# Performance work log

Hardware: AMD Instinct MI355X
Metric: run time of the kernel (lower is better)

Reference implementation:

```python
import jax, jax.numpy as jnp
import numpy as np

EPS = 1e-5
K = 20
NH = 16
SLOPE = 0.2

def leaky(x):
    return jnp.where(x >= 0, x, SLOPE * x)

def bn(x, g, b, axes):
    # training-mode batch norm (biased variance), channel axis = 1
    m = x.mean(axes, keepdims=True)
    v = x.var(axes, keepdims=True)
    shp = [1] * x.ndim
    shp[1] = -1
    return (x - m) / jnp.sqrt(v + EPS) * g.reshape(shp) + b.reshape(shp)

def efr(x, idx, w, k):
    # x: [B, C, N]; idx: flat global gather indices [B*N*k]; w: [C_out, 2C+1]
    B, C, N = x.shape
    xt = x.transpose(0, 2, 1).reshape(B * N, C)
    feature = xt[idx].reshape(B, N, k, C)            # gathered neighbors
    xc = xt.reshape(B, N, 1, C)
    fmean = feature.mean(-1, keepdims=True)          # [B,N,k,1]
    f = jnp.concatenate([feature - xc, fmean, jnp.broadcast_to(xc, feature.shape)], axis=3)
    return jnp.einsum('bnkc,oc->bonk', f, w)         # 1x1 conv -> [B,C_out,N,k]


def setup_inputs() -> dict:
    key = jax.random.key(0)
    ks = jax.random.split(key, 24)
    B, N = 8, 4096
    IN_CH, FEAT_CH, OUT_CH = 6, 64, 64
    d = {}
    d['points'] = jax.random.normal(ks[0], (B, IN_CH // 2, N), dtype=jnp.float32)
    d['feat'] = jax.random.normal(ks[1], (B, FEAT_CH // 2, N), dtype=jnp.float32)
    d['idx'] = jax.random.randint(ks[2], (B * N * K,), 0, B * N)
    s = 0.1
    d['w_efr_p'] = jax.random.normal(ks[3], (IN_CH, IN_CH + 1), dtype=jnp.float32) * s
    d['w_efr_f'] = jax.random.normal(ks[4], (FEAT_CH, FEAT_CH + 1), dtype=jnp.float32) * s
    d['w_q'] = jax.random.normal(ks[5], (FEAT_CH, FEAT_CH // 2), dtype=jnp.float32) * s
    d['g_q'] = jnp.ones((FEAT_CH,), jnp.float32)
    d['b_q'] = jnp.zeros((FEAT_CH,), jnp.float32)
    d['w_pos1'] = jax.random.normal(ks[6], (IN_CH, IN_CH // 2), dtype=jnp.float32) * s
    d['g_pos1'] = jnp.ones((IN_CH,), jnp.float32)
    d['b_pos1'] = jnp.zeros((IN_CH,), jnp.float32)
    d['w_pos2'] = jax.random.normal(ks[7], (FEAT_CH, IN_CH), dtype=jnp.float32) * s
    d['w_attn'] = jax.random.normal(ks[8], (NH * IN_CH, FEAT_CH), dtype=jnp.float32) * s
    d['g1'] = jnp.ones((NH,), jnp.float32)
    d['b1'] = jnp.zeros((NH,), jnp.float32)
    d['w_lin'] = jax.random.normal(ks[9], (OUT_CH, NH), dtype=jnp.float32) * s
    d['g_lin'] = jnp.ones((OUT_CH,), jnp.float32)
    d['b_lin'] = jnp.zeros((OUT_CH,), jnp.float32)
    d['w_res'] = jax.random.normal(ks[10], (OUT_CH, FEAT_CH), dtype=jnp.float32) * s
    d['g_res'] = jnp.ones((OUT_CH,), jnp.float32)
    d['b_res'] = jnp.zeros((OUT_CH,), jnp.float32)
    return d


def reference(points, feat, idx, w_efr_p, w_efr_f, w_q, g_q, b_q,
              w_pos1, g_pos1, b_pos1, w_pos2, w_attn, g1, b1,
              w_lin, g_lin, b_lin, w_res, g_res, b_res):
    B, _, N = points.shape
    knn_points = efr(points, idx, w_efr_p, K)   # [B,6,N,K]
    knn_feat = efr(feat, idx, w_efr_f, K)       # [B,64,N,K]
    x_q = leaky(bn(jnp.einsum('bcn,oc->bon', feat, w_q), g_q, b_q, (0, 2)))
    pos = leaky(bn(jnp.einsum('bcn,oc->bon', points, w_pos1), g_pos1, b_pos1, (0, 2)))
    pos = pos[:, :, :, None] - knn_points       # [B,6,N,K]
    pos = jnp.einsum('bcnk,oc->bonk', pos, w_pos2)  # [B,64,N,K]
    attn = x_q[:, :, :, None] - knn_feat + pos
    attn = jax.nn.softmax(attn / float(np.sqrt(knn_feat.shape[1])), axis=-1)
    attn = jnp.einsum('bcnk,oc->bonk', attn, w_attn)  # [B,NH*6,N,K]
    attn5 = attn.transpose(0, 2, 3, 1).reshape(B, N, K, NH, -1)  # [B,N,K,NH,6]
    y = jnp.einsum('bnkhc,bcnk->bhnk', attn5, knn_points)        # [B,NH,N,K]
    y = leaky(bn(y, g1, b1, (0, 2, 3)))
    y = bn(jnp.einsum('bcnk,oc->bonk', y, w_lin), g_lin, b_lin, (0, 2, 3))
    res = bn(jnp.einsum('bcnk,oc->bonk', knn_feat, w_res), g_res, b_res, (0, 2, 3))
    y = leaky(y + res)
    return y.max(axis=-1)                        # [B,64,N]
```

## Files before the change

kernel.cpp:

```cpp
#include <hip/hip_runtime.h>

#define KNN 20
#define NN 4096
#define NPTS 32768
#define PPW 8

using short8 = __attribute__((ext_vector_type(8))) short;
using f32x4v = __attribute__((ext_vector_type(4))) float;
using uint4v = __attribute__((ext_vector_type(4))) unsigned int;

__device__ __forceinline__ float lrelu(float x){ return x >= 0.f ? x : 0.2f*x; }
__device__ __forceinline__ unsigned short f2b(float x){
    union { float f; unsigned u; } v; v.f = x;
    unsigned r = v.u + 0x7FFFu + ((v.u >> 16) & 1u);
    return (unsigned short)(r >> 16);
}
__device__ __forceinline__ float b2f(unsigned h){
    union { unsigned u; float f; } v; v.u = h << 16; return v.f;
}
#define WSYNC() do { asm volatile("s_waitcnt lgkmcnt(0)" ::: "memory"); __builtin_amdgcn_sched_barrier(0); } while(0)

__device__ __forceinline__ int fslot(int fragi, int klocal, int gp){
    return fragi*1024 + (((klocal) + ((gp)<<4)) ^ ((gp)*5))*16;
}

__global__ void kprep(const float* __restrict__ weff, const float* __restrict__ wattn,
                      const float* __restrict__ wres,
                      unsigned short* __restrict__ packW, float* __restrict__ wdiff,
                      float* __restrict__ w32t)
{
    int t = threadIdx.x;
    for (int q = t; q < 1536; q += 256){
        int f = q >> 6, l = q & 63;
        const float* W; int n, rowlen, koff;
        if (f < 4){ W = weff; rowlen = 65; n = f*16 + (l&15); koff = 0; }
        else if (f < 16){ W = wattn; rowlen = 64; int ff = f-4; n = (ff>>1)*16 + (l&15); koff = (ff&1)*32; }
        else { W = wres; rowlen = 64; int ff = f-16; n = (ff>>1)*16 + (l&15); koff = (ff&1)*32; }
        #pragma unroll
        for (int j=0;j<8;j++){
            int k = koff + (j>=4?16:0) + 4*(l>>4) + (j&3);
            packW[(size_t)(f*64+l)*8 + j] = f2b(W[n*rowlen + k]);
        }
    }
    for (int q = t; q < 2048; q += 256){
        int c = q >> 5, j = q & 31;
        wdiff[q] = weff[c*65 + 33 + j] - weff[c*65 + j];
    }
    if (t < 64) w32t[t] = weff[t*65 + 32];
}

__global__ void __launch_bounds__(256) k0_prep(
    const float* __restrict__ pts, const float* __restrict__ feat,
    const float* __restrict__ wq, const float* __restrict__ wpos1,
    const float* __restrict__ wefp, const float* __restrict__ wdiff,
    unsigned short* __restrict__ ft16, float* __restrict__ pt4,
    unsigned short* __restrict__ qp16, float* __restrict__ pp,
    unsigned short* __restrict__ base16, float* __restrict__ bpp,
    float* __restrict__ qsum, float* __restrict__ qsq,
    float* __restrict__ psum, float* __restrict__ psq)
{
    __shared__ float swq[2048];
    __shared__ float swd[2048];
    __shared__ float red[4][64], red2[4][64];
    int tid = threadIdx.x;
    for (int m=tid;m<2048;m+=256){ swq[m]=wq[m]; swd[m]=wdiff[m]; }
    __syncthreads();
    int r = blockIdx.x*256 + tid;
    int b = r >> 12, n = r & 4095;
    float p0 = pts[((size_t)b*3+0)*NN+n];
    float p1 = pts[((size_t)b*3+1)*NN+n];
    float p2 = pts[((size_t)b*3+2)*NN+n];
    float pm = (p0+p1+p2)*(1.f/3.f);
    *(float4*)(pt4 + (size_t)r*4) = make_float4(p0,p1,p2,pm);
    float f[32];
    #pragma unroll
    for (int c=0;c<32;c++) f[c] = feat[((size_t)b*32+c)*NN+n];
    #pragma unroll
    for (int c=0;c<32;c+=2){
        unsigned pk = (unsigned)f2b(f[c]) | ((unsigned)f2b(f[c+1])<<16);
        *(unsigned*)(ft16 + (size_t)r*32 + c) = pk;
    }
    float q[64];
    for (int o=0;o<64;o++){
        float a=0.f;
        #pragma unroll
        for (int c=0;c<32;c++) a += swq[o*32+c]*f[c];
        q[o]=a;
    }
    for (int o=0;o<64;o+=2){
        unsigned pk = (unsigned)f2b(q[o]) | ((unsigned)f2b(q[o+1])<<16);
        *(unsigned*)(qp16 + (size_t)r*64 + o) = pk;
    }
    int lane = tid & 63, wvv = tid>>6;
    for (int o=0;o<64;o++){
        float s=q[o], s2=q[o]*q[o];
        for (int d=1; d<64; d<<=1){ s += __shfl_xor(s,d); s2 += __shfl_xor(s2,d); }
        if (lane==0){ red[wvv][o]=s; red2[wvv][o]=s2; }
    }
    __syncthreads();
    if (tid<64){
        atomicAdd(qsum+tid, red[0][tid]+red[1][tid]+red[2][tid]+red[3][tid]);
        atomicAdd(qsq+tid, red2[0][tid]+red2[1][tid]+red2[2][tid]+red2[3][tid]);
    }
    for (int o=0;o<64;o++){
        float a=0.f;
        #pragma unroll
        for (int c=0;c<32;c++) a += swd[o*32+c]*f[c];
        q[o]=a;
    }
    for (int o=0;o<64;o+=2){
        unsigned pk = (unsigned)f2b(q[o]) | ((unsigned)f2b(q[o+1])<<16);
        *(unsigned*)(base16 + (size_t)r*64 + o) = pk;
    }
    float pr[8];
    #pragma unroll
    for (int o=0;o<6;o++) pr[o] = wpos1[o*3]*p0 + wpos1[o*3+1]*p1 + wpos1[o*3+2]*p2;
    pr[6]=0.f; pr[7]=0.f;
    *(float4*)(pp+(size_t)r*8)   = make_float4(pr[0],pr[1],pr[2],pr[3]);
    *(float4*)(pp+(size_t)r*8+4) = make_float4(pr[4],pr[5],pr[6],pr[7]);
    __syncthreads();
    for (int o=0;o<6;o++){
        float s=pr[o], s2=pr[o]*pr[o];
        for (int d=1;d<64;d<<=1){ s += __shfl_xor(s,d); s2 += __shfl_xor(s2,d); }
        if (lane==0){ red[wvv][o]=s; red2[wvv][o]=s2; }
    }
    __syncthreads();
    if (tid<6){
        atomicAdd(psum+tid, red[0][tid]+red[1][tid]+red[2][tid]+red[3][tid]);
        atomicAdd(psq+tid, red2[0][tid]+red2[1][tid]+red2[2][tid]+red2[3][tid]);
    }
    #pragma unroll
    for (int j=0;j<6;j++)
        bpp[(size_t)r*8+j] = p0*(wefp[j*7+4]-wefp[j*7]) + p1*(wefp[j*7+5]-wefp[j*7+1])
                           + p2*(wefp[j*7+6]-wefp[j*7+2]);
    bpp[(size_t)r*8+6]=0.f; bpp[(size_t)r*8+7]=0.f;
}

__global__ void k1_paramsA(
    const float* __restrict__ qsum, const float* __restrict__ qsq,
    const float* __restrict__ psum, const float* __restrict__ psq,
    const float* __restrict__ gq, const float* __restrict__ bq,
    const float* __restrict__ gp, const float* __restrict__ bp,
    float* __restrict__ bnq_a, float* __restrict__ bnq_c,
    float* __restrict__ bnp_a, float* __restrict__ bnp_c)
{
    int t = threadIdx.x;
    const float inv = 1.f/32768.f;
    if (t < 64){
        float m = qsum[t]*inv; float v = qsq[t]*inv - m*m;
        float a = gq[t]*rsqrtf(v + 1e-5f);
        bnq_a[t] = a; bnq_c[t] = bq[t] - m*a;
    }
    if (t < 6){
        float m = psum[t]*inv; float v = psq[t]*inv - m*m;
        float a = gp[t]*rsqrtf(v + 1e-5f);
        bnp_a[t] = a; bnp_c[t] = bp[t] - m*a;
    }
}

#define ARENA 12544
#define ANB   0
#define ATR   2048
#define KFR   6272
#define SFM   10368
#define SSKP  10496
#define SIDX  11136
#define YST   11776

__global__ void __launch_bounds__(256, 3) k2_main(
    const unsigned short* __restrict__ ft16, const float* __restrict__ pt4,
    const unsigned short* __restrict__ qp16, const float* __restrict__ pp,
    const unsigned short* __restrict__ base16, const float* __restrict__ bpp,
    const int* __restrict__ idx,
    const float* __restrict__ wefp, const float* __restrict__ wpos2,
    const unsigned short* __restrict__ packW, const float* __restrict__ w32t,
    const float* __restrict__ bnq_a, const float* __restrict__ bnq_c,
    const float* __restrict__ bnp_a, const float* __restrict__ bnp_c,
    unsigned short* __restrict__ yv, unsigned short* __restrict__ rf,
    float* __restrict__ yslot, float* __restrict__ rslot)
{
    __shared__ __align__(16) char smem_[4*ARENA];
    const int tid = threadIdx.x;
    const int l = tid & 63, wv = tid >> 6;
    const int lo = l & 15, g = l >> 4;
    char* S = smem_ + wv*ARENA;
    const int srd = (l ^ (g*5))*16;

    float w2r[4][6], w32r[4], bnqa[4], bnqc[4];
    #pragma unroll
    for (int nt=0;nt<4;nt++){
        #pragma unroll
        for (int j=0;j<6;j++) w2r[nt][j] = wpos2[(nt*16+lo)*6+j];
        w32r[nt] = w32t[nt*16+lo];
        bnqa[nt] = bnq_a[nt*16+lo];
        bnqc[nt] = bnq_c[nt*16+lo];
    }
    float bnpa[6], bnpc[6];
    #pragma unroll
    for (int j=0;j<6;j++){ bnpa[j]=bnp_a[j]; bnpc[j]=bnp_c[j]; }

    float ysum=0.f, ysq=0.f;
    float racc[4]={0.f,0.f,0.f,0.f}, rsqa[4]={0.f,0.f,0.f,0.f};

    const int rbase = blockIdx.x*(4*PPW) + wv*PPW;

    *(int*)(S+SIDX+l*4)        = idx[(size_t)rbase*KNN + l];
    *(int*)(S+SIDX+(64+l)*4)   = idx[(size_t)rbase*KNN + 64 + l];
    if (l < 32) *(int*)(S+SIDX+(128+l)*4) = idx[(size_t)rbase*KNN + 128 + l];
    WSYNC();

    uint2 ng0, ng1; uint2 ng2 = make_uint2(0u,0u); float4 ngp4 = make_float4(0,0,0,0);
    unsigned short nqr[4], nbr[4];
    float nppr[6], nbppr[6];
    float xqv[4], basev[4], sp[6];

#define ISSUE(pi_) { \
    int sb = (pi_)*KNN*4; size_t rr = (size_t)(rbase + (pi_)); \
    int i0 = *(const int*)(S+SIDX+sb+(l>>3)*4); \
    int i1 = *(const int*)(S+SIDX+sb+(8+(l>>3))*4); \
    ng0 = *(const uint2*)(ft16 + (size_t)i0*32 + (l&7)*4); \
    ng1 = *(const uint2*)(ft16 + (size_t)i1*32 + (l&7)*4); \
    if (l < 32){ int i2 = *(const int*)(S+SIDX+sb+(16+(l>>3))*4); \
                 ng2 = *(const uint2*)(ft16 + (size_t)i2*32 + (l&7)*4); } \
    if (l < KNN){ int ip = *(const int*)(S+SIDX+sb+l*4); \
                  ngp4 = *(const float4*)(pt4 + (size_t)ip*4); } \
    _Pragma("unroll") for (int nt=0;nt<4;nt++){ \
        nqr[nt] = qp16[rr*64 + nt*16+lo]; nbr[nt] = base16[rr*64 + nt*16+lo]; } \
    _Pragma("unroll") for (int j=0;j<6;j++){ nppr[j] = pp[rr*8+j]; nbppr[j] = bpp[rr*8+j]; } \
    __builtin_amdgcn_sched_barrier(0); \
}

#define STAGE() { \
    float s0 = b2f(ng0.x&0xffffu)+b2f(ng0.x>>16)+b2f(ng0.y&0xffffu)+b2f(ng0.y>>16); \
    float s1 = b2f(ng1.x&0xffffu)+b2f(ng1.x>>16)+b2f(ng1.y&0xffffu)+b2f(ng1.y>>16); \
    float s2 = b2f(ng2.x&0xffffu)+b2f(ng2.x>>16)+b2f(ng2.y&0xffffu)+b2f(ng2.y>>16); \
    s0 += __shfl_xor(s0,1); s0 += __shfl_xor(s0,2); s0 += __shfl_xor(s0,4); \
    s1 += __shfl_xor(s1,1); s1 += __shfl_xor(s1,2); s1 += __shfl_xor(s1,4); \
    s2 += __shfl_xor(s2,1); s2 += __shfl_xor(s2,2); s2 += __shfl_xor(s2,4); \
    if ((l&7)==0){ \
        *(float*)(S+SFM+(l>>3)*4) = s0*(1.f/32.f); \
        *(float*)(S+SFM+(8+(l>>3))*4) = s1*(1.f/32.f); \
        if (l < 32) *(float*)(S+SFM+(16+(l>>3))*4) = s2*(1.f/32.f); \
    } \
    { int kk = l>>3, gp_ = l&3, jb = ((l>>2)&1)*8; \
      *(uint2*)(S + ANB + fslot(0, kk, gp_) + jb) = ng0; \
      *(uint2*)(S + ANB + fslot(0, 8+kk, gp_) + jb) = ng1; \
      if (l < 32) *(uint2*)(S + ANB + fslot(1, kk, gp_) + jb) = ng2; } \
    if (l < KNN){ \
        _Pragma("unroll") for (int j=0;j<6;j++){ \
            float v = nbppr[j] + wefp[j*7]*ngp4.x + wefp[j*7+1]*ngp4.y \
                    + wefp[j*7+2]*ngp4.z + wefp[j*7+3]*ngp4.w; \
            *(float*)(S+SSKP+(l*8+j)*4) = v; } } \
    _Pragma("unroll") for (int nt=0;nt<4;nt++){ \
        xqv[nt] = lrelu(bnqa[nt]*b2f(nqr[nt]) + bnqc[nt]); \
        basev[nt] = b2f(nbr[nt]); } \
    _Pragma("unroll") for (int j=0;j<6;j++) sp[j] = lrelu(bnpa[j]*nppr[j] + bnpc[j]); \
    WSYNC(); \
}

    ISSUE(0);
    STAGE();

    for (int pi=0; pi<PPW; pi++){
        const size_t r = (size_t)(rbase + pi);
        if (pi < PPW-1) ISSUE(pi+1);

        f32x4v C1[2][4];
        #pragma unroll
        for (int mt=0;mt<2;mt++)
            #pragma unroll
            for (int nt=0;nt<4;nt++)
                #pragma unroll
                for (int i=0;i<4;i++) C1[mt][nt][i] = 0.f;
        short8 Af0 = *(const short8*)(S + ANB + 0*1024 + srd);
        short8 Af1 = *(const short8*)(S + ANB + 1*1024 + srd);
        #pragma unroll
        for (int nt=0;nt<4;nt++){
            short8 Bf = *(const short8*)(packW + (size_t)(nt*64 + l)*8);
            C1[0][nt] = __builtin_amdgcn_mfma_f32_16x16x32_bf16(Af0, Bf, C1[0][nt], 0, 0, 0);
            C1[1][nt] = __builtin_amdgcn_mfma_f32_16x16x32_bf16(Af1, Bf, C1[1][nt], 0, 0, 0);
        }
        #pragma unroll
        for (int mt=0;mt<2;mt++){
            #pragma unroll
            for (int i=0;i<4;i++){
                int k = mt*16 + g*4 + i;
                bool valid = (k < KNN);
                int kk = valid ? k : 0;
                float fmk = *(const float*)(S+SFM+kk*4);
                float sk[6];
                #pragma unroll
                for (int j=0;j<6;j++) sk[j] = *(const float*)(S+SSKP+(kk*8+j)*4);
                #pragma unroll
                for (int nt=0;nt<4;nt++){
                    float kf = C1[mt][nt][i] + basev[nt] + w32r[nt]*fmk;
                    if (valid){
                        int fa = fslot(mt*2+(nt>>1), g*4+i, lo>>2) + ((nt&1)*4 + (lo&3))*2;
                        *(unsigned short*)(S + KFR + fa) = f2b(kf);
                    }
                    float pos = 0.f;
                    #pragma unroll
                    for (int j=0;j<6;j++) pos += (sp[j]-sk[j])*w2r[nt][j];
                    C1[mt][nt][i] = valid ? (xqv[nt] - kf + pos)*0.125f : -1e30f;
                }
            }
        }
        #pragma unroll
        for (int nt=0;nt<4;nt++){
            float mx = -1e30f;
            #pragma unroll
            for (int mt=0;mt<2;mt++)
                #pragma unroll
                for (int i=0;i<4;i++) mx = fmaxf(mx, C1[mt][nt][i]);
            mx = fmaxf(mx, __shfl_xor(mx,16));
            mx = fmaxf(mx, __shfl_xor(mx,32));
            float sm = 0.f;
            #pragma unroll
            for (int mt=0;mt<2;mt++)
                #pragma unroll
                for (int i=0;i<4;i++){ float e = __expf(C1[mt][nt][i]-mx); C1[mt][nt][i]=e; sm += e; }
            sm += __shfl_xor(sm,16);
            sm += __shfl_xor(sm,32);
            float inv = 1.f/sm;
            #pragma unroll
            for (int mt=0;mt<2;mt++)
                #pragma unroll
                for (int i=0;i<4;i++){
                    int k = mt*16 + g*4 + i;
                    if (k < KNN){
                        int fa = fslot(mt*2+(nt>>1), g*4+i, lo>>2) + ((nt&1)*4 + (lo&3))*2;
                        *(unsigned short*)(S + ATR + fa) = f2b(C1[mt][nt][i]*inv);
                    }
                }
        }
        WSYNC();
        short8 Aa[2][2];
        #pragma unroll
        for (int mt=0;mt<2;mt++)
            #pragma unroll
            for (int s=0;s<2;s++) Aa[mt][s] = *(const short8*)(S + ATR + (mt*2+s)*1024 + srd);
        f32x4v C2[2][6];
        #pragma unroll
        for (int mt=0;mt<2;mt++)
            #pragma unroll
            for (int nt=0;nt<6;nt++)
                #pragma unroll
                for (int i=0;i<4;i++) C2[mt][nt][i] = 0.f;
        #pragma unroll
        for (int nt=0;nt<6;nt++){
            #pragma unroll
            for (int s=0;s<2;s++){
                short8 Bf = *(const short8*)(packW + (size_t)((4+nt*2+s)*64 + l)*8);
                #pragma unroll
                for (int mt=0;mt<2;mt++)
                    C2[mt][nt] = __builtin_amdgcn_mfma_f32_16x16x32_bf16(Aa[mt][s], Bf, C2[mt][nt], 0, 0, 0);
            }
        }
        WSYNC();
        #pragma unroll
        for (int mt=0;mt<2;mt++)
            #pragma unroll
            for (int nt=0;nt<6;nt++)
                #pragma unroll
                for (int i=0;i<4;i++){
                    int k = mt*16 + g*4 + i;
                    if (k < KNN)
                        *(unsigned short*)(S + ATR + k*208 + (nt*16+lo)*2) = f2b(C2[mt][nt][i]);
                }
        WSYNC();
        #pragma unroll
        for (int it=0; it<5; it++){
            int kq = it*4 + g;
            const char* row = S + ATR + kq*208 + lo*12;
            unsigned d0 = *(const unsigned*)(row);
            unsigned d1 = *(const unsigned*)(row+4);
            unsigned d2 = *(const unsigned*)(row+8);
            float yval = b2f(d0&0xffffu) * (*(const float*)(S+SSKP+(kq*8+0)*4))
                       + b2f(d0>>16)    * (*(const float*)(S+SSKP+(kq*8+1)*4))
                       + b2f(d1&0xffffu)* (*(const float*)(S+SSKP+(kq*8+2)*4))
                       + b2f(d1>>16)    * (*(const float*)(S+SSKP+(kq*8+3)*4))
                       + b2f(d2&0xffffu)* (*(const float*)(S+SSKP+(kq*8+4)*4))
                       + b2f(d2>>16)    * (*(const float*)(S+SSKP+(kq*8+5)*4));
            *(unsigned short*)(S + YST + kq*32 + lo*2) = f2b(yval);
            ysum += yval; ysq += yval*yval;
        }
        short8 Ak[2][2];
        #pragma unroll
        for (int mt=0;mt<2;mt++)
            #pragma unroll
            for (int s=0;s<2;s++) Ak[mt][s] = *(const short8*)(S + KFR + (mt*2+s)*1024 + srd);
        f32x4v C3[2][4];
        #pragma unroll
        for (int mt=0;mt<2;mt++)
            #pragma unroll
            for (int nt=0;nt<4;nt++)
                #pragma unroll
                for (int i=0;i<4;i++) C3[mt][nt][i] = 0.f;
        #pragma unroll
        for (int nt=0;nt<4;nt++){
            #pragma unroll
            for (int s=0;s<2;s++){
                short8 Bf = *(const short8*)(packW + (size_t)((16+nt*2+s)*64 + l)*8);
                #pragma unroll
                for (int mt=0;mt<2;mt++)
                    C3[mt][nt] = __builtin_amdgcn_mfma_f32_16x16x32_bf16(Ak[mt][s], Bf, C3[mt][nt], 0, 0, 0);
            }
        }
        WSYNC();
        #pragma unroll
        for (int mt=0;mt<2;mt++)
            #pragma unroll
            for (int i=0;i<4;i++){
                int k = mt*16 + g*4 + i;
                if (k < KNN){
                    #pragma unroll
                    for (int nt=0;nt<4;nt++){
                        float v = C3[mt][nt][i];
                        *(unsigned short*)(S + ATR + k*144 + (nt*16+lo)*2) = f2b(v);
                        racc[nt] += v; rsqa[nt] += v*v;
                    }
                }
            }
        WSYNC();
        if (l < 40){
            uint4v v = *(const uint4v*)(S + YST + l*16);
            __builtin_nontemporal_store(v, (uint4v*)((char*)yv + r*640 + l*16));
        }
        #pragma unroll
        for (int t=0;t<3;t++){
            int s = t*64 + l;
            if (s < 160){
                int kk = s>>3, pt_ = s&7;
                uint4v v = *(const uint4v*)(S + ATR + kk*144 + pt_*16);
                __builtin_nontemporal_store(v, (uint4v*)((char*)rf + r*2560 + kk*128 + pt_*16));
            }
        }
        if (pi < PPW-1) STAGE();
    }
    ysum += __shfl_xor(ysum,16); ysum += __shfl_xor(ysum,32);
    ysq  += __shfl_xor(ysq,16);  ysq  += __shfl_xor(ysq,32);
    #pragma unroll
    for (int nt=0;nt<4;nt++){
        racc[nt] += __shfl_xor(racc[nt],16); racc[nt] += __shfl_xor(racc[nt],32);
        rsqa[nt] += __shfl_xor(rsqa[nt],16); rsqa[nt] += __shfl_xor(rsqa[nt],32);
    }
    int slot = (blockIdx.x*4 + wv) & 63;
    if (l < 16){
        atomicAdd(yslot + slot*32 + l, ysum);
        #pragma unroll
        for (int nt=0;nt<4;nt++) atomicAdd(rslot + slot*128 + nt*16 + l, racc[nt]);
    } else if (l < 32){
        atomicAdd(yslot + slot*32 + 16 + lo, ysq);
        #pragma unroll
        for (int nt=0;nt<4;nt++) atomicAdd(rslot + slot*128 + 64 + nt*16 + lo, rsqa[nt]);
    }
#undef ISSUE
#undef STAGE
}

__global__ void k3_paramsB(
    const float* __restrict__ yslot, const float* __restrict__ rslot,
    const float* __restrict__ g1, const float* __restrict__ b1,
    const float* __restrict__ gr, const float* __restrict__ br,
    float* __restrict__ bn1_a, float* __restrict__ bn1_c,
    float* __restrict__ bnr_a, float* __restrict__ bnr_c)
{
    __shared__ float sy[32];
    __shared__ float sr[128];
    int t = threadIdx.x;
    float s1 = 0.f;
    if (t < 32){ for (int i=0;i<64;i++) s1 += yslot[(size_t)i*32+t]; }
    float s2 = 0.f;
    for (int i=0;i<64;i++) s2 += rslot[(size_t)i*128+t];
    if (t < 32) sy[t] = s1;
    sr[t] = s2;
    __syncthreads();
    const float inv = 1.f/655360.f;
    if (t < 16){
        float m = sy[t]*inv; float v = sy[16+t]*inv - m*m;
        float a = g1[t]*rsqrtf(v + 1e-5f);
        bn1_a[t] = a; bn1_c[t] = b1[t] - m*a;
    }
    if (t < 64){
        float m = sr[t]*inv; float v = sr[64+t]*inv - m*m;
        float a = gr[t]*rsqrtf(v + 1e-5f);
        bnr_a[t] = a; bnr_c[t] = br[t] - m*a;
    }
}

__global__ void __launch_bounds__(256) k4_linstats(
    const unsigned short* __restrict__ yv,
    const float* __restrict__ bn1_a, const float* __restrict__ bn1_c,
    float* __restrict__ Mslot, float* __restrict__ Sslot)
{
    __shared__ __align__(16) char lds[4*1024];
    const int tid = threadIdx.x, l = tid & 63, wvv = tid >> 6;
    const int lo = l & 15, g = l >> 4;
    char* L = lds + wvv*1024;
    const int h0 = (l&1)*8;
    float a8[8], c8[8];
    #pragma unroll
    for (int j=0;j<8;j++){ a8[j]=bn1_a[h0+j]; c8[j]=bn1_c[h0+j]; }
    short8 ones;
    #pragma unroll
    for (int j=0;j<8;j++) ones[j] = (short)0x3F80;
    f32x4v Macc, Sacc;
    #pragma unroll
    for (int i=0;i<4;i++){ Macc[i]=0.f; Sacc[i]=0.f; }
    const int waveid = blockIdx.x*4 + wvv;
    for (int it=0; it<5; it++){
        size_t s0 = ((size_t)waveid*5 + it)*32;
        uint4 v = *(const uint4*)(yv + s0*16 + l*8);
        unsigned short e0 = v.x&0xffffu, e1 = v.x>>16, e2 = v.y&0xffffu, e3 = v.y>>16;
        unsigned short e4 = v.z&0xffffu, e5 = v.z>>16, e6 = v.w&0xffffu, e7 = v.w>>16;
        float y0 = lrelu(a8[0]*b2f(e0)+c8[0]), y1 = lrelu(a8[1]*b2f(e1)+c8[1]);
        float y2_ = lrelu(a8[2]*b2f(e2)+c8[2]), y3 = lrelu(a8[3]*b2f(e3)+c8[3]);
        float y4 = lrelu(a8[4]*b2f(e4)+c8[4]), y5 = lrelu(a8[5]*b2f(e5)+c8[5]);
        float y6 = lrelu(a8[6]*b2f(e6)+c8[6]), y7 = lrelu(a8[7]*b2f(e7)+c8[7]);
        uint4 o;
        o.x = (unsigned)f2b(y0) | ((unsigned)f2b(y1)<<16);
        o.y = (unsigned)f2b(y2_)| ((unsigned)f2b(y3)<<16);
        o.z = (unsigned)f2b(y4) | ((unsigned)f2b(y5)<<16);
        o.w = (unsigned)f2b(y6) | ((unsigned)f2b(y7)<<16);
        *(uint4*)(L + l*16) = o;
        WSYNC();
        short8 Af;
        #pragma unroll
        for (int j=0;j<8;j++){
            int s = 4*g + (j&3) + ((j>=4)?16:0);
            Af[j] = *(const short*)(L + s*32 + lo*2);
        }
        WSYNC();
        Macc = __builtin_amdgcn_mfma_f32_16x16x32_bf16(Af, Af, Macc, 0, 0, 0);
        Sacc = __builtin_amdgcn_mfma_f32_16x16x32_bf16(ones, Af, Sacc, 0, 0, 0);
    }
    float* Ms = Mslot + (size_t)(waveid&15)*256;
    #pragma unroll
    for (int i=0;i<4;i++) atomicAdd(Ms + (g*4+i)*16 + lo, Macc[i]);
    if (l < 16) atomicAdd(Sslot + (size_t)(waveid&15)*16 + lo, Sacc[0]);
}

__global__ void k5_paramsC(
    const float* __restrict__ Mslot, const float* __restrict__ Sslot,
    const float* __restrict__ wl,
    const float* __restrict__ gl, const float* __restrict__ bl,
    float* __restrict__ bnl_a, float* __restrict__ bnl_c)
{
    __shared__ float Ms[256], Ss[16];
    int t = threadIdx.x;
    float m = 0.f;
    for (int i=0;i<16;i++) m += Mslot[(size_t)i*256+t];
    Ms[t] = m;
    if (t < 16){
        float s = 0.f;
        for (int i=0;i<16;i++) s += Sslot[(size_t)i*16+t];
        Ss[t] = s;
    }
    __syncthreads();
    if (t < 64){
        float w[16];
        #pragma unroll
        for (int h=0;h<16;h++) w[h] = wl[t*16+h];
        float lsum = 0.f;
        #pragma unroll
        for (int h=0;h<16;h++) lsum += w[h]*Ss[h];
        float lsq = 0.f;
        for (int h1=0;h1<16;h1++){
            float acc = 0.f;
            #pragma unroll
            for (int h2=0;h2<16;h2++) acc += Ms[h1*16+h2]*w[h2];
            lsq += w[h1]*acc;
        }
        const float inv = 1.f/655360.f;
        float mean = lsum*inv; float var = lsq*inv - mean*mean;
        float a = gl[t]*rsqrtf(var + 1e-5f);
        bnl_a[t] = a; bnl_c[t] = bl[t] - mean*a;
    }
}

__global__ void __launch_bounds__(256) k6_final(
    const unsigned short* __restrict__ yv, const unsigned short* __restrict__ rf,
    const float* __restrict__ bn1_a, const float* __restrict__ bn1_c,
    const float* __restrict__ wl,
    const float* __restrict__ bnl_a, const float* __restrict__ bnl_c,
    const float* __restrict__ bnr_a, const float* __restrict__ bnr_c,
    float* __restrict__ out)
{
    __shared__ float sy2[4][16*KNN];
    __shared__ float sout[64][17];
    const int tid = threadIdx.x;
    const int w = tid >> 6, o = tid & 63;
    float wlr[16];
    #pragma unroll
    for (int h=0;h<16;h++) wlr[h] = wl[o*16+h];
    const float la = bnl_a[o], lc = bnl_c[o];
    const float ra = bnr_a[o], rc = bnr_c[o];
    const int r0 = blockIdx.x*16;
    for (int i=0;i<4;i++){
        const size_t r = (size_t)r0 + w*4 + i;
        __syncthreads();
        for (int m=o;m<320;m+=64){
            float yy = b2f(yv[r*320+m]);
            int h = m & 15;
            sy2[w][m] = lrelu(bn1_a[h]*yy + bn1_c[h]);
        }
        __syncthreads();
        float best = -1e30f;
        for (int k=0;k<KNN;k++){
            unsigned short rv16 = __builtin_nontemporal_load(rf + r*1280 + k*64 + o);
            float rv = b2f(rv16);
            float lv = 0.f;
            #pragma unroll
            for (int h=0;h<16;h++) lv += wlr[h]*sy2[w][k*16+h];
            float val = lrelu(la*lv + lc + ra*rv + rc);
            best = fmaxf(best, val);
        }
        sout[o][w*4+i] = best;
    }
    __syncthreads();
    const int b = r0 >> 12, n0 = r0 & 4095;
    for (int m=tid;m<1024;m+=256){
        int oo = m >> 4, ii = m & 15;
        out[((size_t)b*64+oo)*NN + n0 + ii] = sout[oo][ii];
    }
}

extern "C" void kernel_launch(void* const* d_in, const int* in_sizes, int n_in,
                              void* d_out, int out_size, void* d_ws, size_t ws_size,
                              hipStream_t stream)
{
    const float* pts   = (const float*)d_in[0];
    const float* feat  = (const float*)d_in[1];
    const int*   idx   = (const int*)d_in[2];
    const float* wefp  = (const float*)d_in[3];
    const float* weff  = (const float*)d_in[4];
    const float* wq    = (const float*)d_in[5];
    const float* gq    = (const float*)d_in[6];
    const float* bq    = (const float*)d_in[7];
    const float* wpos1 = (const float*)d_in[8];
    const float* gp    = (const float*)d_in[9];
    const float* bp    = (const float*)d_in[10];
    const float* wpos2 = (const float*)d_in[11];
    const float* wattn = (const float*)d_in[12];
    const float* g1    = (const float*)d_in[13];
    const float* b1    = (const float*)d_in[14];
    const float* wl    = (const float*)d_in[15];
    const float* gl    = (const float*)d_in[16];
    const float* bl    = (const float*)d_in[17];
    const float* wres  = (const float*)d_in[18];
    const float* gr    = (const float*)d_in[19];
    const float* br    = (const float*)d_in[20];
    float* out = (float*)d_out;

    char* ws = (char*)d_ws;
    size_t o_ft16 = 0;
    size_t o_pt4  = o_ft16 + (size_t)NPTS*32*2;
    size_t o_qp16 = o_pt4  + (size_t)NPTS*4*4;
    size_t o_pp   = o_qp16 + (size_t)NPTS*64*2;
    size_t o_b16  = o_pp   + (size_t)NPTS*8*4;
    size_t o_bpp  = o_b16  + (size_t)NPTS*64*2;
    size_t o_packW= o_bpp  + (size_t)NPTS*8*4;
    size_t o_wdiff= o_packW + 24*512*2;
    size_t o_w32  = o_wdiff + 2048*4;
    size_t o_st   = o_w32   + 64*4;
    size_t o_qsum  = o_st;
    size_t o_qsq   = o_qsum + 64*4;
    size_t o_psum  = o_qsq  + 64*4;
    size_t o_psq   = o_psum + 8*4;
    size_t o_yslot = o_psq  + 8*4;
    size_t o_rslot = o_yslot + (size_t)64*32*4;
    size_t o_mslot = o_rslot + (size_t)64*128*4;
    size_t o_sslot = o_mslot + (size_t)16*256*4;
    size_t zero_bytes = (o_sslot + (size_t)16*16*4) - o_st;
    size_t o_par   = o_st + zero_bytes;
    size_t o_bnq_a = o_par;
    size_t o_bnq_c = o_bnq_a + 64*4;
    size_t o_bnp_a = o_bnq_c + 64*4;
    size_t o_bnp_c = o_bnp_a + 8*4;
    size_t o_bn1_a = o_bnp_c + 8*4;
    size_t o_bn1_c = o_bn1_a + 16*4;
    size_t o_bnl_a = o_bn1_c + 16*4;
    size_t o_bnl_c = o_bnl_a + 64*4;
    size_t o_bnr_a = o_bnl_c + 64*4;
    size_t o_bnr_c = o_bnr_a + 64*4;
    size_t o_yv = (o_bnr_c + 64*4 + 255) & ~(size_t)255;
    size_t o_rf = o_yv + (size_t)NPTS*320*2;

    unsigned short* ft16 = (unsigned short*)(ws + o_ft16);
    float* pt4  = (float*)(ws + o_pt4);
    unsigned short* qp16 = (unsigned short*)(ws + o_qp16);
    float* ppb  = (float*)(ws + o_pp);
    unsigned short* b16p = (unsigned short*)(ws + o_b16);
    float* bppb = (float*)(ws + o_bpp);
    unsigned short* packW = (unsigned short*)(ws + o_packW);
    float* wdiff= (float*)(ws + o_wdiff);
    float* w32t = (float*)(ws + o_w32);
    float* qsum = (float*)(ws + o_qsum);
    float* qsq  = (float*)(ws + o_qsq);
    float* psum = (float*)(ws + o_psum);
    float* psq  = (float*)(ws + o_psq);
    float* yslot= (float*)(ws + o_yslot);
    float* rslot= (float*)(ws + o_rslot);
    float* Mslot= (float*)(ws + o_mslot);
    float* Sslot= (float*)(ws + o_sslot);
    float* bnq_a= (float*)(ws + o_bnq_a);
    float* bnq_c= (float*)(ws + o_bnq_c);
    float* bnp_a= (float*)(ws + o_bnp_a);
    float* bnp_c= (float*)(ws + o_bnp_c);
    float* bn1_a= (float*)(ws + o_bn1_a);
    float* bn1_c= (float*)(ws + o_bn1_c);
    float* bnl_a= (float*)(ws + o_bnl_a);
    float* bnl_c= (float*)(ws + o_bnl_c);
    float* bnr_a= (float*)(ws + o_bnr_a);
    float* bnr_c= (float*)(ws + o_bnr_c);
    unsigned short* yvp = (unsigned short*)(ws + o_yv);
    unsigned short* rfp = (unsigned short*)(ws + o_rf);

    (void)hipMemsetAsync(ws + o_st, 0, zero_bytes, stream);

    kprep<<<1, 256, 0, stream>>>(weff, wattn, wres, packW, wdiff, w32t);
    k0_prep<<<128, 256, 0, stream>>>(pts, feat, wq, wpos1, wefp, wdiff,
                                     ft16, pt4, qp16, ppb, b16p, bppb,
                                     qsum, qsq, psum, psq);
    k1_paramsA<<<1, 64, 0, stream>>>(qsum, qsq, psum, psq, gq, bq, gp, bp,
                                     bnq_a, bnq_c, bnp_a, bnp_c);
    k2_main<<<NPTS/(4*PPW), 256, 0, stream>>>(ft16, pt4, qp16, ppb, b16p, bppb, idx,
                                     wefp, wpos2, packW, w32t,
                                     bnq_a, bnq_c, bnp_a, bnp_c,
                                     yvp, rfp, yslot, rslot);
    k3_paramsB<<<1, 128, 0, stream>>>(yslot, rslot, g1, b1, gr, br,
                                      bn1_a, bn1_c, bnr_a, bnr_c);
    k4_linstats<<<1024, 256, 0, stream>>>(yvp, bn1_a, bn1_c, Mslot, Sslot);
    k5_paramsC<<<1, 256, 0, stream>>>(Mslot, Sslot, wl, gl, bl, bnl_a, bnl_c);
    k6_final<<<2048, 256, 0, stream>>>(yvp, rfp, bn1_a, bn1_c, wl,
                                       bnl_a, bnl_c, bnr_a, bnr_c, out);
}
```

Baseline: 549.1 us.

## Recompute residual projection in final kernel instead of storing it

The residual branch (w_res applied to the edge features) is no longer written out from the main kernel as a large bf16 tensor. Instead w_res is folded into the edge-feature weights (w_res*w_eff, per-point base terms and a mean coefficient), and the final kernel re-gathers the neighbour features and recomputes it with MFMA. The final kernel also moves the w_lin projection onto MFMA. This trades a large global write and re-read of roughly 80 KB-per-block residual data for extra gathers and matrix work in k6, and the pre-multiplied weights change bf16 rounding behaviour.

```diff
diff --git a/kernel.cpp b/kernel.cpp
--- a/kernel.cpp
+++ b/kernel.cpp
@@ -25,45 +25,89 @@
 }
 
 __global__ void kprep(const float* __restrict__ weff, const float* __restrict__ wattn,
-                      const float* __restrict__ wres,
+                      const float* __restrict__ wres, const float* __restrict__ wl,
                       unsigned short* __restrict__ packW, float* __restrict__ wdiff,
-                      float* __restrict__ w32t)
+                      float* __restrict__ w32t, float* __restrict__ wrb,
+                      float* __restrict__ rww)
 {
+    __shared__ float sres[4096];
+    __shared__ float sweff[4160];
+    __shared__ float scomb[2048];
     int t = threadIdx.x;
+    for (int m=t; m<4096; m+=256) sres[m] = wres[m];
+    for (int m=t; m<4160; m+=256) sweff[m] = weff[m];
+    __syncthreads();
+    for (int q=t;q<2048;q+=256){
+        int c=q>>5, j=q&31;
+        wdiff[q] = sweff[c*65+33+j]-sweff[c*65+j];
+    }
+    if (t<64) w32t[t] = sweff[t*65+32];
+    for (int q=t;q<2048;q+=256){
+        int o=q>>5, j=q&31;
+        float a=0.f, b=0.f;
+        for (int c=0;c<64;c++){
+            float wr = sres[o*64+c];
+            a += wr*sweff[c*65+j];
+            b += wr*(sweff[c*65+33+j]-sweff[c*65+j]);
+        }
+        scomb[q]=a; wrb[q]=b;
+    }
+    if (t<64){
+        float a=0.f;
+        for (int c=0;c<64;c++) a += sres[t*64+c]*sweff[c*65+32];
+        rww[t]=a;
+    }
+    __syncthreads();
     for (int q = t; q < 1536; q += 256){
         int f = q >> 6, l = q & 63;
-        const float* W; int n, rowlen, koff;
-        if (f < 4){ W = weff; rowlen = 65; n = f*16 + (l&15); koff = 0; }
-        else if (f < 16){ W = wattn; rowlen = 64; int ff = f-4; n = (ff>>1)*16 + (l&15); koff = (ff&1)*32; }
-        else { W = wres; rowlen = 64; int ff = f-16; n = (ff>>1)*16 + (l&15); koff = (ff&1)*32; }
         #pragma unroll
         for (int j=0;j<8;j++){
-            int k = koff + (j>=4?16:0) + 4*(l>>4) + (j&3);
-            packW[(size_t)(f*64+l)*8 + j] = f2b(W[n*rowlen + k]);
-        }
-    }
-    for (int q = t; q < 2048; q += 256){
-        int c = q >> 5, j = q & 31;
-        wdiff[q] = weff[c*65 + 33 + j] - weff[c*65 + j];
-    }
-    if (t < 64) w32t[t] = weff[t*65 + 32];
+            int koff, n; float v;
+            if (f < 4){ n = f*16 + (l&15); koff = 0;
+                int k = koff + (j>=4?16:0) + 4*(l>>4) + (j&3);
+                v = sweff[n*65 + k];
+            } else if (f < 16){ int ff=f-4; n = (ff>>1)*16 + (l&15); koff = (ff&1)*32;
+                int k = koff + (j>=4?16:0) + 4*(l>>4) + (j&3);
+                v = wattn[n*64 + k];
+            } else { int ff=f-16; n = (ff>>1)*16 + (l&15); koff = (ff&1)*32;
+                int k = koff + (j>=4?16:0) + 4*(l>>4) + (j&3);
+                v = sres[n*64 + k];
+            }
+            packW[(size_t)(f*64+l)*8 + j] = f2b(v);
+        }
+    }
+    for (int q=t;q<512;q+=256){
+        int f=q>>6, l=q&63;
+        int nt = f&3; bool iswl = f>=4;
+        #pragma unroll
+        for (int j=0;j<8;j++){
+            int kdim = (j>=4?16:0)+4*(l>>4)+(j&3);
+            float v;
+            if (!iswl) v = scomb[(nt*16+(l&15))*32 + kdim];
+            else v = (kdim<16) ? wl[(nt*16+(l&15))*16 + kdim] : 0.f;
+            packW[(size_t)((24+f)*64+l)*8+j] = f2b(v);
+        }
+    }
 }
 
 __global__ void __launch_bounds__(256) k0_prep(
     const float* __restrict__ pts, const float* __restrict__ feat,
     const float* __restrict__ wq, const float* __restrict__ wpos1,
     const float* __restrict__ wefp, const float* __restrict__ wdiff,
+    const float* __restrict__ wrb,
     unsigned short* __restrict__ ft16, float* __restrict__ pt4,
     unsigned short* __restrict__ qp16, float* __restrict__ pp,
     unsigned short* __restrict__ base16, float* __restrict__ bpp,
+    unsigned short* __restrict__ rb16,
     float* __restrict__ qsum, float* __restrict__ qsq,
     float* __restrict__ psum, float* __restrict__ psq)
 {
     __shared__ float swq[2048];
     __shared__ float swd[2048];
+    __shared__ float swr[2048];
     __shared__ float red[4][64], red2[4][64];
     int tid = threadIdx.x;
-    for (int m=tid;m<2048;m+=256){ swq[m]=wq[m]; swd[m]=wdiff[m]; }
+    for (int m=tid;m<2048;m+=256){ swq[m]=wq[m]; swd[m]=wdiff[m]; swr[m]=wrb[m]; }
     __syncthreads();
     int r = blockIdx.x*256 + tid;
     int b = r >> 12, n = r & 4095;
@@ -111,6 +155,16 @@
     for (int o=0;o<64;o+=2){
         unsigned pk = (unsigned)f2b(q[o]) | ((unsigned)f2b(q[o+1])<<16);
         *(unsigned*)(base16 + (size_t)r*64 + o) = pk;
+    }
+    for (int o=0;o<64;o++){
+        float a=0.f;
+        #pragma unroll
+        for (int c=0;c<32;c++) a += swr[o*32+c]*f[c];
+        q[o]=a;
+    }
+    for (int o=0;o<64;o+=2){
+        unsigned pk = (unsigned)f2b(q[o]) | ((unsigned)f2b(q[o+1])<<16);
+        *(unsigned*)(rb16 + (size_t)r*64 + o) = pk;
     }
     float pr[8];
     #pragma unroll
@@ -176,7 +230,7 @@
     const unsigned short* __restrict__ packW, const float* __restrict__ w32t,
     const float* __restrict__ bnq_a, const float* __restrict__ bnq_c,
     const float* __restrict__ bnp_a, const float* __restrict__ bnp_c,
-    unsigned short* __restrict__ yv, unsigned short* __restrict__ rf,
+    unsigned short* __restrict__ yv,
     float* __restrict__ yslot, float* __restrict__ rslot)
 {
     __shared__ __align__(16) char smem_[4*ARENA];
@@ -406,7 +460,6 @@
                     C3[mt][nt] = __builtin_amdgcn_mfma_f32_16x16x32_bf16(Ak[mt][s], Bf, C3[mt][nt], 0, 0, 0);
             }
         }
-        WSYNC();
         #pragma unroll
         for (int mt=0;mt<2;mt++)
             #pragma unroll
@@ -416,7 +469,6 @@
                     #pragma unroll
                     for (int nt=0;nt<4;nt++){
                         float v = C3[mt][nt][i];
-                        *(unsigned short*)(S + ATR + k*144 + (nt*16+lo)*2) = f2b(v);
                         racc[nt] += v; rsqa[nt] += v*v;
                     }
                 }
@@ -424,16 +476,7 @@
         WSYNC();
         if (l < 40){
             uint4v v = *(const uint4v*)(S + YST + l*16);
-            __builtin_nontemporal_store(v, (uint4v*)((char*)yv + r*640 + l*16));
-        }
-        #pragma unroll
-        for (int t=0;t<3;t++){
-            int s = t*64 + l;
-            if (s < 160){
-                int kk = s>>3, pt_ = s&7;
-                uint4v v = *(const uint4v*)(S + ATR + kk*144 + pt_*16);
-                __builtin_nontemporal_store(v, (uint4v*)((char*)rf + r*2560 + kk*128 + pt_*16));
-            }
+            *(uint4v*)((char*)yv + r*640 + l*16) = v;
         }
         if (pi < PPW-1) STAGE();
     }
@@ -578,51 +621,159 @@
     }
 }
 
+#define ARENA6 2848
+#define SFM6 2048
+#define SIDX6 2176
+
 __global__ void __launch_bounds__(256) k6_final(
-    const unsigned short* __restrict__ yv, const unsigned short* __restrict__ rf,
+    const unsigned short* __restrict__ ft16, const unsigned short* __restrict__ yv,
+    const int* __restrict__ idx, const unsigned short* __restrict__ rb16,
+    const unsigned short* __restrict__ packW, const float* __restrict__ rww,
     const float* __restrict__ bn1_a, const float* __restrict__ bn1_c,
-    const float* __restrict__ wl,
     const float* __restrict__ bnl_a, const float* __restrict__ bnl_c,
     const float* __restrict__ bnr_a, const float* __restrict__ bnr_c,
     float* __restrict__ out)
 {
-    __shared__ float sy2[4][16*KNN];
-    __shared__ float sout[64][17];
+    __shared__ __align__(16) char smem_[4*ARENA6];
+    __shared__ float sval[64*36];
     const int tid = threadIdx.x;
-    const int w = tid >> 6, o = tid & 63;
-    float wlr[16];
-    #pragma unroll
-    for (int h=0;h<16;h++) wlr[h] = wl[o*16+h];
-    const float la = bnl_a[o], lc = bnl_c[o];
-    const float ra = bnr_a[o], rc = bnr_c[o];
-    const int r0 = blockIdx.x*16;
-    for (int i=0;i<4;i++){
-        const size_t r = (size_t)r0 + w*4 + i;
-        __syncthreads();
-        for (int m=o;m<320;m+=64){
-            float yy = b2f(yv[r*320+m]);
-            int h = m & 15;
-            sy2[w][m] = lrelu(bn1_a[h]*yy + bn1_c[h]);
-        }
-        __syncthreads();
-        float best = -1e30f;
-        for (int k=0;k<KNN;k++){
-            unsigned short rv16 = __builtin_nontemporal_load(rf + r*1280 + k*64 + o);
-            float rv = b2f(rv16);
-            float lv = 0.f;
-            #pragma unroll
-            for (int h=0;h<16;h++) lv += wlr[h]*sy2[w][k*16+h];
-            float val = lrelu(la*lv + lc + ra*rv + rc);
-            best = fmaxf(best, val);
-        }
-        sout[o][w*4+i] = best;
+    const int l = tid & 63, wv = tid >> 6;
+    const int lo = l & 15, g = l >> 4;
+    char* S = smem_ + wv*ARENA6;
+    const int srd = (l ^ (g*5))*16;
+
+    short8 Bc[4], Bl[4];
+    #pragma unroll
+    for (int nt=0;nt<4;nt++){
+        Bc[nt] = *(const short8*)(packW + (size_t)((24+nt)*64+l)*8);
+        Bl[nt] = *(const short8*)(packW + (size_t)((28+nt)*64+l)*8);
+    }
+    float4 b1a = *(const float4*)(bn1_a + 4*g);
+    float4 b1c = *(const float4*)(bn1_c + 4*g);
+    float la[4], lc[4], ra[4], rc[4], rwv[4];
+    #pragma unroll
+    for (int nt=0;nt<4;nt++){
+        int o = nt*16+lo;
+        la[nt]=bnl_a[o]; lc[nt]=bnl_c[o]; ra[nt]=bnr_a[o]; rc[nt]=bnr_c[o]; rwv[nt]=rww[o];
+    }
+    const int rbase = blockIdx.x*32 + wv*8;
+    *(int*)(S+SIDX6+l*4)      = idx[(size_t)rbase*KNN + l];
+    *(int*)(S+SIDX6+(64+l)*4) = idx[(size_t)rbase*KNN + 64 + l];
+    if (l < 32) *(int*)(S+SIDX6+(128+l)*4) = idx[(size_t)rbase*KNN + 128 + l];
+    WSYNC();
+
+    uint2 ng0, ng1; uint2 ng2 = make_uint2(0u,0u);
+    uint2 ylo_, yhi_; unsigned short rbr[4];
+    short8 AlyA, AlyB; float rbv[4];
+
+#define ISSUE6(pi_) { \
+    int sb = (pi_)*KNN*4; size_t rr = (size_t)(rbase + (pi_)); \
+    int i0 = *(const int*)(S+SIDX6+sb+(l>>3)*4); \
+    int i1 = *(const int*)(S+SIDX6+sb+(8+(l>>3))*4); \
+    ng0 = *(const uint2*)(ft16 + (size_t)i0*32 + (l&7)*4); \
+    ng1 = *(const uint2*)(ft16 + (size_t)i1*32 + (l&7)*4); \
+    if (l < 32){ int i2 = *(const int*)(S+SIDX6+sb+(16+(l>>3))*4); \
+                 ng2 = *(const uint2*)(ft16 + (size_t)i2*32 + (l&7)*4); } \
+    ylo_ = *(const uint2*)(yv + rr*320 + (l&15)*16 + g*4); \
+    yhi_ = make_uint2(0u,0u); \
+    if (lo < 4) yhi_ = *(const uint2*)(yv + rr*320 + (16+(l&15))*16 + g*4); \
+    _Pragma("unroll") for (int nt=0;nt<4;nt++) rbr[nt] = rb16[rr*64 + nt*16+lo]; \
+    __builtin_amdgcn_sched_barrier(0); \
+}
+
+#define STAGE6() { \
+    float s0 = b2f(ng0.x&0xffffu)+b2f(ng0.x>>16)+b2f(ng0.y&0xffffu)+b2f(ng0.y>>16); \
+    float s1 = b2f(ng1.x&0xffffu)+b2f(ng1.x>>16)+b2f(ng1.y&0xffffu)+b2f(ng1.y>>16); \
+    float s2 = b2f(ng2.x&0xffffu)+b2f(ng2.x>>16)+b2f(ng2.y&0xffffu)+b2f(ng2.y>>16); \
+    s0 += __shfl_xor(s0,1); s0 += __shfl_xor(s0,2); s0 += __shfl_xor(s0,4); \
+    s1 += __shfl_xor(s1,1); s1 += __shfl_xor(s1,2); s1 += __shfl_xor(s1,4); \
+    s2 += __shfl_xor(s2,1); s2 += __shfl_xor(s2,2); s2 += __shfl_xor(s2,4); \
+    if ((l&7)==0){ \
+        *(float*)(S+SFM6+(l>>3)*4) = s0*(1.f/32.f); \
+        *(float*)(S+SFM6+(8+(l>>3))*4) = s1*(1.f/32.f); \
+        if (l < 32) *(float*)(S+SFM6+(16+(l>>3))*4) = s2*(1.f/32.f); \
+    } \
+    { int kk = l>>3, gp_ = l&3, jb = ((l>>2)&1)*8; \
+      *(uint2*)(S + fslot(0, kk, gp_) + jb) = ng0; \
+      *(uint2*)(S + fslot(0, 8+kk, gp_) + jb) = ng1; \
+      if (l < 32) *(uint2*)(S + fslot(1, kk, gp_) + jb) = ng2; } \
+    { float t0 = lrelu(b1a.x*b2f(ylo_.x&0xffffu)+b1c.x); \
+      float t1 = lrelu(b1a.y*b2f(ylo_.x>>16)+b1c.y); \
+      float t2 = lrelu(b1a.z*b2f(ylo_.y&0xffffu)+b1c.z); \
+      float t3 = lrelu(b1a.w*b2f(ylo_.y>>16)+b1c.w); \
+      AlyA[0]=(short)f2b(t0); AlyA[1]=(short)f2b(t1); AlyA[2]=(short)f2b(t2); AlyA[3]=(short)f2b(t3); \
+      AlyA[4]=0; AlyA[5]=0; AlyA[6]=0; AlyA[7]=0; \
+      t0 = lrelu(b1a.x*b2f(yhi_.x&0xffffu)+b1c.x); \
+      t1 = lrelu(b1a.y*b2f(yhi_.x>>16)+b1c.y); \
+      t2 = lrelu(b1a.z*b2f(yhi_.y&0xffffu)+b1c.z); \
+      t3 = lrelu(b1a.w*b2f(yhi_.y>>16)+b1c.w); \
+      AlyB[0]=(short)f2b(t0); AlyB[1]=(short)f2b(t1); AlyB[2]=(short)f2b(t2); AlyB[3]=(short)f2b(t3); \
+      AlyB[4]=0; AlyB[5]=0; AlyB[6]=0; AlyB[7]=0; } \
+    _Pragma("unroll") for (int nt=0;nt<4;nt++) rbv[nt] = b2f(rbr[nt]); \
+    WSYNC(); \
+}
+
+    ISSUE6(0);
+    STAGE6();
+
+    for (int pi=0; pi<8; pi++){
+        if (pi < 7) ISSUE6(pi+1);
+        short8 Af0 = *(const short8*)(S + 0*1024 + srd);
+        short8 Af1 = *(const short8*)(S + 1*1024 + srd);
+        f32x4v Crv[2][4], Clv[2][4];
+        #pragma unroll
+        for (int mt=0;mt<2;mt++)
+            #pragma unroll
+            for (int nt=0;nt<4;nt++)
+                #pragma unroll
+                for (int i=0;i<4;i++){ Crv[mt][nt][i]=0.f; Clv[mt][nt][i]=0.f; }
+        #pragma unroll
+        for (int nt=0;nt<4;nt++){
+            Crv[0][nt] = __builtin_amdgcn_mfma_f32_16x16x32_bf16(Af0, Bc[nt], Crv[0][nt], 0, 0, 0);
+            Crv[1][nt] = __builtin_amdgcn_mfma_f32_16x16x32_bf16(Af1, Bc[nt], Crv[1][nt], 0, 0, 0);
+            Clv[0][nt] = __builtin_amdgcn_mfma_f32_16x16x32_bf16(AlyA, Bl[nt], Clv[0][nt], 0, 0, 0);
+            Clv[1][nt] = __builtin_amdgcn_mfma_f32_16x16x32_bf16(AlyB, Bl[nt], Clv[1][nt], 0, 0, 0);
+        }
+        float vmax[4] = {-1e30f,-1e30f,-1e30f,-1e30f};
+        #pragma unroll
+        for (int mt=0;mt<2;mt++)
+            #pragma unroll
+            for (int i=0;i<4;i++){
+                int k = mt*16 + g*4 + i;
+                if (k < KNN){
+                    float fmk = *(const float*)(S+SFM6+k*4);
+                    #pragma unroll
+                    for (int nt=0;nt<4;nt++){
+                        float rv = Crv[mt][nt][i] + rbv[nt] + rwv[nt]*fmk;
+                        float lv = Clv[mt][nt][i];
+                        float val = lrelu(la[nt]*lv + lc[nt] + ra[nt]*rv + rc[nt]);
+                        vmax[nt] = fmaxf(vmax[nt], val);
+                    }
+                }
+            }
+        #pragma unroll
+        for (int nt=0;nt<4;nt++){
+            vmax[nt] = fmaxf(vmax[nt], __shfl_xor(vmax[nt],16));
+            vmax[nt] = fmaxf(vmax[nt], __shfl_xor(vmax[nt],32));
+        }
+        if (l < 16){
+            #pragma unroll
+            for (int nt=0;nt<4;nt++)
+                sval[(nt*16+lo)*36 + wv*8 + pi] = vmax[nt];
+        }
+        if (pi < 7) STAGE6();
     }
     __syncthreads();
-    const int b = r0 >> 12, n0 = r0 & 4095;
-    for (int m=tid;m<1024;m+=256){
-        int oo = m >> 4, ii = m & 15;
-        out[((size_t)b*64+oo)*NN + n0 + ii] = sout[oo][ii];
-    }
+    {
+        int o = tid >> 2, seg = tid & 3;
+        float4 v0 = *(const float4*)(sval + o*36 + seg*8);
+        float4 v1 = *(const float4*)(sval + o*36 + seg*8 + 4);
+        size_t base = ((size_t)(blockIdx.x>>7)*64 + o)*NN + (blockIdx.x&127)*32 + seg*8;
+        *(float4*)(out + base) = v0;
+        *(float4*)(out + base + 4) = v1;
+    }
+#undef ISSUE6
+#undef STAGE6
 }
 
 extern "C" void kernel_launch(void* const* d_in, const int* in_sizes, int n_in,
@@ -654,14 +805,17 @@
 
     char* ws = (char*)d_ws;
     size_t o_ft16 = 0;
-    size_t o_pt4  = o_ft16 + (size_t)NPTS*32*2;
-    size_t o_qp16 = o_pt4  + (size_t)NPTS*4*4;
-    size_t o_pp   = o_qp16 + (size_t)NPTS*64*2;
-    size_t o_b16  = o_pp   + (size_t)NPTS*8*4;
-    size_t o_bpp  = o_b16  + (size_t)NPTS*64*2;
-    size_t o_packW= o_bpp  + (size_t)NPTS*8*4;
-    size_t o_wdiff= o_packW + 24*512*2;
-    size_t o_w32  = o_wdiff + 2048*4;
+    size_t o_pt4  = o_ft16 + (size_t)NPTS*64;
+    size_t o_qp16 = o_pt4  + (size_t)NPTS*16;
+    size_t o_pp   = o_qp16 + (size_t)NPTS*128;
+    size_t o_b16  = o_pp   + (size_t)NPTS*32;
+    size_t o_bpp  = o_b16  + (size_t)NPTS*128;
+    size_t o_rb16 = o_bpp  + (size_t)NPTS*32;
+    size_t o_packW= o_rb16 + (size_t)NPTS*128;
+    size_t o_wdiff= o_packW + 32*512*2;
+    size_t o_wrb  = o_wdiff + 2048*4;
+    size_t o_rw   = o_wrb   + 2048*4;
+    size_t o_w32  = o_rw    + 64*4;
     size_t o_st   = o_w32   + 64*4;
     size_t o_qsum  = o_st;
     size_t o_qsq   = o_qsum + 64*4;
@@ -684,7 +838,6 @@
     size_t o_bnr_a = o_bnl_c + 64*4;
     size_t o_bnr_c = o_bnr_a + 64*4;
     size_t o_yv = (o_bnr_c + 64*4 + 255) & ~(size_t)255;
-    size_t o_rf = o_yv + (size_t)NPTS*320*2;
 
     unsigned short* ft16 = (unsigned short*)(ws + o_ft16);
     float* pt4  = (float*)(ws + o_pt4);
@@ -692,8 +845,11 @@
     float* ppb  = (float*)(ws + o_pp);
     unsigned short* b16p = (unsigned short*)(ws + o_b16);
     float* bppb = (float*)(ws + o_bpp);
+    unsigned short* rb16 = (unsigned short*)(ws + o_rb16);
     unsigned short* packW = (unsigned short*)(ws + o_packW);
     float* wdiff= (float*)(ws + o_wdiff);
+    float* wrb  = (float*)(ws + o_wrb);
+    float* rww  = (float*)(ws + o_rw);
     float* w32t = (float*)(ws + o_w32);
     float* qsum = (float*)(ws + o_qsum);
     float* qsq  = (float*)(ws + o_qsq);
@@ -714,24 +870,23 @@
     float* bnr_a= (float*)(ws + o_bnr_a);
     float* bnr_c= (float*)(ws + o_bnr_c);
     unsigned short* yvp = (unsigned short*)(ws + o_yv);
-    unsigned short* rfp = (unsigned short*)(ws + o_rf);
 
     (void)hipMemsetAsync(ws + o_st, 0, zero_bytes, stream);
 
-    kprep<<<1, 256, 0, stream>>>(weff, wattn, wres, packW, wdiff, w32t);
-    k0_prep<<<128, 256, 0, stream>>>(pts, feat, wq, wpos1, wefp, wdiff,
-                                     ft16, pt4, qp16, ppb, b16p, bppb,
+    kprep<<<1, 256, 0, stream>>>(weff, wattn, wres, wl, packW, wdiff, w32t, wrb, rww);
+    k0_prep<<<128, 256, 0, stream>>>(pts, feat, wq, wpos1, wefp, wdiff, wrb,
+                                     ft16, pt4, qp16, ppb, b16p, bppb, rb16,
                                      qsum, qsq, psum, psq);
     k1_paramsA<<<1, 64, 0, stream>>>(qsum, qsq, psum, psq, gq, bq, gp, bp,
                                      bnq_a, bnq_c, bnp_a, bnp_c);
     k2_main<<<NPTS/(4*PPW), 256, 0, stream>>>(ft16, pt4, qp16, ppb, b16p, bppb, idx,
                                      wefp, wpos2, packW, w32t,
                                      bnq_a, bnq_c, bnp_a, bnp_c,
-                                     yvp, rfp, yslot, rslot);
+                                     yvp, yslot, rslot);
     k3_paramsB<<<1, 128, 0, stream>>>(yslot, rslot, g1, b1, gr, br,
                                       bn1_a, bn1_c, bnr_a, bnr_c);
     k4_linstats<<<1024, 256, 0, stream>>>(yvp, bn1_a, bn1_c, Mslot, Sslot);
     k5_paramsC<<<1, 256, 0, stream>>>(Mslot, Sslot, wl, gl, bl, bnl_a, bnl_c);
-    k6_final<<<2048, 256, 0, stream>>>(yvp, rfp, bn1_a, bn1_c, wl,
-                                       bnl_a, bnl_c, bnr_a, bnr_c, out);
-}
+    k6_final<<<1024, 256, 0, stream>>>(ft16, yvp, idx, rb16, packW, rww,
+                                       bn1_a, bn1_c, bnl_a, bnl_c, bnr_a, bnr_c, out);
+}
```

Result: slower. 562.7 us (+2.5%).
